# Kernel tuning notes

Measured on AMD Instinct MI355X. Metric: run time of the kernel, lower is better.

Reference implementation:

```python
import jax, jax.numpy as jnp
import numpy as np

NEIGHBOUR_NUM = 8  # args.neighbour_num


def _sqrdis_map(x, y):
    # x: [B,M,3], y: [B,N,3] -> [B,M,N] squared distances
    x2 = jnp.sum(x * x, axis=-1)
    y2 = jnp.sum(y * y, axis=-1)
    inner = jnp.einsum('bmd,bnd->bmn', x, y)
    return x2[:, :, None] + y2[:, None, :] - 2.0 * inner


def _chamfer(x, y):
    d = _sqrdis_map(x, y)
    return d.min(axis=2), d.min(axis=1)


def _neighbor_index(v, k):
    # torch.topk(dist, k+1, largest=False) then drop self
    d = _sqrdis_map(v, v)
    idx = jax.lax.top_k(-d, k + 1)[1]  # ascending distance order
    return idx[:, :, 1:]


def _arap(idx, dp, sp):
    B = dp.shape[0]
    bid = jnp.arange(B)[:, None, None]
    dn = dp[bid, idx] - dp[:, :, None, :]  # [B,N,K,3]
    sn = sp[bid, idx] - sp[:, :, None, :]
    dd = jnp.sqrt(jnp.sum(dn * dn, axis=-1) + 1e-5)
    sd = jnp.sqrt(jnp.sum(sn * sn, axis=-1) + 1e-5)
    diff = dd - sd
    return jnp.sum(diff * diff) / B


def setup_inputs() -> dict:
    key = jax.random.key(0)
    ks = jax.random.split(key, 7)
    T, B, N = 3, 4, 4096
    return {
        'phi': jax.random.normal(ks[0], (T, B, 1024), dtype=jnp.float32),
        'point_weight': jax.random.normal(ks[1], (T, B, N, 1), dtype=jnp.float32),
        'deform_rigid_points': 0.5 * jax.random.normal(ks[2], (T, B, N, 3), dtype=jnp.float32),
        'deformation_points': 0.5 * jax.random.normal(ks[3], (T, B, N, 3), dtype=jnp.float32),
        'rigid_matrix': 0.1 * jax.random.normal(ks[4], (T, B, 4, 4), dtype=jnp.float32),
        'source_points': jax.random.uniform(ks[5], (B, N, 3), dtype=jnp.float32, minval=-1.0, maxval=1.0),
        'target_points': jax.random.uniform(ks[6], (B, N, 3), dtype=jnp.float32, minval=-1.0, maxval=1.0),
    }


def reference(phi, point_weight, deform_rigid_points, deformation_points,
              rigid_matrix, source_points, target_points):
    B = source_points.shape[0]
    T = phi.shape[0]  # iter_time = len(phi_list)
    idx = _neighbor_index(source_points, NEIGHBOUR_NUM)
    trans_mask = jnp.zeros((4, 4), dtype=rigid_matrix.dtype).at[0:3, 3].set(1.0)
    total = jnp.asarray(0.0, dtype=source_points.dtype)
    for t in range(T):  # small fixed iter count, structurally distinct stages
        dp = deformation_points[t]
        # loss_on_cd
        d1, d2 = _chamfer(dp, target_points)
        cd = (jnp.sum(d1) + jnp.sum(d2)) * 0.5 / B
        # loss_on_pd (rigid-deformed vs full deformation)
        diff = deform_rigid_points[t] - dp
        pd = jnp.sum(diff * diff) / B
        # loss_on_sparse
        sp = jnp.mean(jnp.abs(point_weight[t]))
        # loss_on_tran
        tr = trans_mask[None] * rigid_matrix[t]
        tran = jnp.sum(tr * tr) / B
        # loss_on_arap
        ar = _arap(idx, dp, source_points)
        total = total + cd + pd + sp + tran + ar
    return total
```

## Files before the change

kernel.cpp:

```cpp
#include <hip/hip_runtime.h>

#define T_ 3
#define B_ 4
#define N_ 4096
#define K_ 8

#define GROUPS 32
#define GRP_KNN 32
#define GRP_CH  12
#define GRP_SZ  45
#define CWIN 512

typedef short bf16x8 __attribute__((ext_vector_type(8)));
typedef float f32x4  __attribute__((ext_vector_type(4)));

template <int NW>
__device__ inline float block_reduce(float v, float* scratch) {
    #pragma unroll
    for (int off = 32; off > 0; off >>= 1) v += __shfl_down(v, off, 64);
    const int lane = threadIdx.x & 63, wid = threadIdx.x >> 6;
    if (lane == 0) scratch[wid] = v;
    __syncthreads();
    float s = 0.f;
    if (threadIdx.x == 0) {
        #pragma unroll
        for (int w = 0; w < NW; ++w) s += scratch[w];
    }
    return s;
}

#define CE_(A, i, j) { unsigned lo_ = min(A[i], A[j]); A[j] = max(A[i], A[j]); A[i] = lo_; }
__device__ inline void sort8(unsigned s[8]) {
    CE_(s,0,1) CE_(s,2,3) CE_(s,4,5) CE_(s,6,7)
    CE_(s,0,2) CE_(s,1,3) CE_(s,4,6) CE_(s,5,7)
    CE_(s,1,2) CE_(s,5,6)
    CE_(s,0,4) CE_(s,1,5) CE_(s,2,6) CE_(s,3,7)
    CE_(s,2,4) CE_(s,3,5)
    CE_(s,1,2) CE_(s,3,4) CE_(s,5,6)
}
__device__ inline void merge_top8(unsigned a[8], const unsigned s[8]) {
    #pragma unroll
    for (int i = 0; i < 8; ++i) a[i] = min(a[i], s[7 - i]);
    CE_(a,0,4) CE_(a,1,5) CE_(a,2,6) CE_(a,3,7)
    CE_(a,0,2) CE_(a,1,3) CE_(a,4,6) CE_(a,5,7)
    CE_(a,0,1) CE_(a,2,3) CE_(a,4,5) CE_(a,6,7)
}

__device__ inline short hi16(float v) { return (short)(__float_as_uint(v) >> 16); }
__device__ inline float residual(float v) {
    return v - __uint_as_float(__float_as_uint(v) & 0xFFFF0000u);
}
__device__ inline unsigned pk2(short a, short b) {
    return (unsigned)(unsigned short)a | ((unsigned)(unsigned short)b << 16);
}
#define BF16_ONE ((short)0x3F80)

__global__ __launch_bounds__(256, 6) void mega_kernel(const float* __restrict__ src,
                                                      const float* __restrict__ dp_all,
                                                      const float* __restrict__ tp,
                                                      const float* __restrict__ drp,
                                                      const float* __restrict__ pw,
                                                      const float* __restrict__ rm,
                                                      float* __restrict__ out) {
    __shared__ uint4 smem4[1024];
    const f32x4 zero4 = {0.f, 0.f, 0.f, 0.f};

    const int g = blockIdx.x / GRP_SZ;
    const int r = blockIdx.x % GRP_SZ;

    if (r < GRP_KNN) {
        const int knn_id = g * GRP_KNN + r;
        uint4* alds = smem4;
        const int b   = knn_id / (N_ / 16);
        const int qt0 = (knn_id % (N_ / 16)) * 16;
        const float* sb = src + (size_t)b * N_ * 3;

        const int wid  = __builtin_amdgcn_readfirstlane(threadIdx.x >> 6);
        const int lane = threadIdx.x & 63;
        const int n    = lane & 15;
        const int quad = lane >> 4;
        const int rbase = quad * 4;
        const int qid  = qt0 + n;

        bf16x8 bfrag = (bf16x8)(short)0;
        {
            float x = sb[3 * qid], y = sb[3 * qid + 1], z = sb[3 * qid + 2];
            float q2 = fmaf(x, x, fmaf(y, y, z * z));
            short hx = hi16(x), hy = hi16(y), hz = hi16(z);
            short lx = hi16(residual(x)), ly = hi16(residual(y)), lz = hi16(residual(z));
            if (quad == 0) bfrag = (bf16x8){hx, hy, hz, hx, hy, hz, BF16_ONE, BF16_ONE};
            else if (quad == 1) bfrag = (bf16x8){lx, ly, lz, lx, ly, lz,
                                                 hi16(q2), hi16(residual(q2))};
        }

        unsigned a[K_];
        #pragma unroll
        for (int p = 0; p < K_; ++p) a[p] = 0xFFFFFFFFu;

        for (int w = 0; w < N_ / CWIN; ++w) {
            __syncthreads();
            #pragma unroll
            for (int rr = 0; rr < 2; ++rr) {
                int jloc = rr * 256 + threadIdx.x;
                int jg = w * CWIN + jloc;
                float x = sb[3 * jg], y = sb[3 * jg + 1], z = sb[3 * jg + 2];
                float p2 = fmaf(x, x, fmaf(y, y, z * z));
                float mx = -2.f * x, my = -2.f * y, mz = -2.f * z;
                short mhx = hi16(mx), mhy = hi16(my), mhz = hi16(mz);
                short mlx = hi16(residual(mx)), mly = hi16(residual(my)), mlz = hi16(residual(mz));
                uint4 f0 = make_uint4(pk2(mhx, mhy), pk2(mhz, mlx), pk2(mly, mlz),
                                      pk2(hi16(p2), hi16(residual(p2))));
                uint4 f1 = make_uint4(f0.x, f0.y, f0.z, pk2(BF16_ONE, BF16_ONE));
                int tile = jloc >> 4, m = jloc & 15;
                alds[tile * 32 + m]      = f0;
                alds[tile * 32 + 16 + m] = f1;
            }
            __syncthreads();

            #pragma unroll
            for (int bt = 0; bt < 4; ++bt) {
                unsigned s8[8];
                #pragma unroll
                for (int h = 0; h < 2; ++h) {
                    const int tile = wid * 8 + bt * 2 + h;
                    const int tbg  = w * CWIN + tile * 16;
                    bf16x8 af = (bf16x8)(short)0;
                    if (quad < 2) {
                        union { uint4 u; bf16x8 v; } cv;
                        cv.u = alds[tile * 32 + quad * 16 + n];
                        af = cv.v;
                    }
                    f32x4 d = __builtin_amdgcn_mfma_f32_16x16x32_bf16(af, bfrag, zero4, 0, 0, 0);
                    #pragma unroll
                    for (int rr = 0; rr < 4; ++rr)
                        s8[h * 4 + rr] = (__float_as_uint(d[rr]) & 0xFFFFF000u)
                                         | (unsigned)(tbg | (rbase + rr));
                    if (tbg == qt0) {
                        #pragma unroll
                        for (int rr = 0; rr < 4; ++rr)
                            if (rbase + rr == n) s8[h * 4 + rr] = 0xFFFFFFFFu;
                    }
                }
                sort8(s8);
                merge_top8(a, s8);
            }
        }

        #pragma unroll
        for (int mk = 16; mk <= 32; mk <<= 1) {
            unsigned t[8];
            #pragma unroll
            for (int e = 0; e < K_; ++e) t[e] = __shfl_xor(a[e], mk, 64);
            merge_top8(a, t);
        }

        __syncthreads();
        unsigned* sm = (unsigned*)smem4;
        unsigned* nidx = (unsigned*)smem4 + 1024;
        if (lane < 16) {
            #pragma unroll
            for (int e = 0; e < K_; ++e) sm[(wid * 16 + n) * 9 + e] = a[e];
        }
        __syncthreads();
        if (threadIdx.x < 16) {
            const int q = threadIdx.x;
            unsigned md[K_];
            #pragma unroll
            for (int e = 0; e < K_; ++e) md[e] = sm[q * 9 + e];
            #pragma unroll
            for (int wv = 1; wv < 4; ++wv) {
                unsigned t[8];
                #pragma unroll
                for (int e = 0; e < K_; ++e) t[e] = sm[(wv * 16 + q) * 9 + e];
                merge_top8(md, t);
            }
            #pragma unroll
            for (int e = 0; e < K_; ++e) nidx[q * 8 + e] = md[e] & 0xFFFu;
        }
        __syncthreads();

        float acc = 0.f;
        if (threadIdx.x < 16 * K_) {
            const int q  = threadIdx.x >> 3;
            const int qi = qt0 + q;
            const int j  = (int)nidx[threadIdx.x];
            float sx = sb[3 * qi], sy = sb[3 * qi + 1], sz = sb[3 * qi + 2];
            float ex = sb[3 * j] - sx, ey = sb[3 * j + 1] - sy, ez = sb[3 * j + 2] - sz;
            float sd = sqrtf(fmaf(ex, ex, fmaf(ey, ey, ez * ez)) + 1e-5f);
            #pragma unroll
            for (int t = 0; t < T_; ++t) {
                const float* dpb = dp_all + ((size_t)(t * B_ + b)) * N_ * 3;
                float dx = dpb[3 * j] - dpb[3 * qi];
                float dy = dpb[3 * j + 1] - dpb[3 * qi + 1];
                float dz = dpb[3 * j + 2] - dpb[3 * qi + 2];
                float dd = sqrtf(fmaf(dx, dx, fmaf(dy, dy, dz * dz)) + 1e-5f);
                float df = dd - sd;
                acc = fmaf(df, df, acc);
            }
        }
        float s = block_reduce<4>(acc, (float*)smem4);
        if (threadIdx.x == 0) atomicAdd(out, s * (1.0f / B_));

    } else if (r < GRP_KNN + GRP_CH) {
        const int cb = g * GRP_CH + (r - GRP_KNN);
        uint4* alds = smem4;
        const int tbd  = cb >> 4;
        const int slab = cb & 15;
        const int dir = tbd & 1;
        const int tb  = tbd >> 1;
        const int b = tb % B_, t = tb / B_;

        const float* dpb = dp_all + ((size_t)(t * B_ + b)) * N_ * 3;
        const float* tpb = tp + (size_t)b * N_ * 3;
        const float* cbase = dir ? dpb : tpb;
        const float* qbase = dir ? tpb : dpb;

        const int lane = threadIdx.x & 63;
        const int wave = threadIdx.x >> 6;
        const int quad = lane >> 4;
        const int n    = lane & 15;

        bf16x8 bfrag[4];
        float  q2r[4];
        #pragma unroll
        for (int s = 0; s < 4; ++s) {
            int qid = slab * 256 + wave * 64 + s * 16 + n;
            float x = qbase[3 * qid], y = qbase[3 * qid + 1], z = qbase[3 * qid + 2];
            q2r[s] = fmaf(x, x, fmaf(y, y, z * z));
            short hx = hi16(x), hy = hi16(y), hz = hi16(z);
            short lx = hi16(residual(x)), ly = hi16(residual(y)), lz = hi16(residual(z));
            if (quad == 0)
                bfrag[s] = (bf16x8){hx, hy, hz, hx, hy, hz, BF16_ONE, BF16_ONE};
            else if (quad == 1)
                bfrag[s] = (bf16x8){lx, ly, lz, lx, ly, lz, 0, 0};
            else
                bfrag[s] = (bf16x8)(short)0;
        }

        float run[4] = {3.4e38f, 3.4e38f, 3.4e38f, 3.4e38f};

        for (int w = 0; w < N_ / CWIN; ++w) {
            __syncthreads();
            #pragma unroll
            for (int rr = 0; rr < 2; ++rr) {
                int jloc = rr * 256 + threadIdx.x;
                int jg = w * CWIN + jloc;
                float x = cbase[3 * jg], y = cbase[3 * jg + 1], z = cbase[3 * jg + 2];
                float p2 = fmaf(x, x, fmaf(y, y, z * z));
                float mx = -2.f * x, my = -2.f * y, mz = -2.f * z;
                short mhx = hi16(mx), mhy = hi16(my), mhz = hi16(mz);
                short mlx = hi16(residual(mx)), mly = hi16(residual(my)), mlz = hi16(residual(mz));
                uint4 f0 = make_uint4(pk2(mhx, mhy), pk2(mhz, mlx), pk2(mly, mlz),
                                      pk2(hi16(p2), hi16(residual(p2))));
                uint4 f1 = make_uint4(f0.x, f0.y, f0.z, 0u);
                int tile = jloc >> 4, m = jloc & 15;
                alds[tile * 32 + m]      = f0;
                alds[tile * 32 + 16 + m] = f1;
            }
            __syncthreads();

            #pragma unroll 4
            for (int tile = 0; tile < CWIN / 16; ++tile) {
                bf16x8 af = (bf16x8)(short)0;
                if (quad < 2) {
                    union { uint4 u; bf16x8 v; } cv;
                    cv.u = alds[tile * 32 + quad * 16 + n];
                    af = cv.v;
                }
                #pragma unroll
                for (int s = 0; s < 4; ++s) {
                    f32x4 d = __builtin_amdgcn_mfma_f32_16x16x32_bf16(af, bfrag[s], zero4, 0, 0, 0);
                    float r3 = fminf(fminf(d[0], d[1]), d[2]);
                    run[s] = fminf(fminf(run[s], r3), d[3]);
                }
            }
        }

        float vsum = 0.f;
        #pragma unroll
        for (int s = 0; s < 4; ++s) {
            float rr = run[s];
            rr = fminf(rr, __shfl_xor(rr, 32));
            rr = fminf(rr, __shfl_xor(rr, 16));
            if (lane < 16) vsum += rr + q2r[s];
        }
        __syncthreads();
        float ssum = block_reduce<4>(vsum, (float*)smem4);
        if (threadIdx.x == 0) atomicAdd(out, ssum * (0.5f / B_));

    } else {
        const int PD_N = T_ * B_ * N_ * 3;
        const int SP_N = T_ * B_ * N_;
        const int stride = GROUPS * 256;
        const int gid = g * 256 + threadIdx.x;
        float apd = 0.f;
        for (int i = gid; i < PD_N; i += stride) {
            float d = drp[i] - dp_all[i];
            apd = fmaf(d, d, apd);
        }
        float asp = 0.f;
        for (int i = gid; i < SP_N; i += stride) asp += fabsf(pw[i]);
        float atr = 0.f;
        if (gid < T_ * B_ * 3) {
            int t = gid / (B_ * 3);
            int b = (gid / 3) % B_;
            int rr = gid % 3;
            float v = rm[t * B_ * 16 + b * 16 + rr * 4 + 3];
            atr = v * v;
        }
        float acc = apd * (1.0f / B_) + asp * (1.0f / (B_ * N_)) + atr * (1.0f / B_);
        float s = block_reduce<4>(acc, (float*)smem4);
        if (threadIdx.x == 0) atomicAdd(out, s);
    }
}

extern "C" void kernel_launch(void* const* d_in, const int* in_sizes, int n_in,
                              void* d_out, int out_size, void* d_ws, size_t ws_size,
                              hipStream_t stream) {
    const float* pw  = (const float*)d_in[1];
    const float* drp = (const float*)d_in[2];
    const float* dp  = (const float*)d_in[3];
    const float* rm  = (const float*)d_in[4];
    const float* sp  = (const float*)d_in[5];
    const float* tp  = (const float*)d_in[6];
    float* out = (float*)d_out;

    hipMemsetAsync(out, 0, sizeof(float), stream);
    mega_kernel<<<GROUPS * GRP_SZ, 256, 0, stream>>>(sp, dp, tp, drp, pw, rm, out);
}
```

Measured before the change: 122.8 us.

## Switch chamfer MFMA to 32x32x16 and fold query norm into K

The chamfer branch moves from 16x16x32 bf16 MFMAs, where half of the K dimension was zero padding, to 32x32x16 MFMAs with a fully packed K. The hi/lo split coordinates, the candidate norm and the query norm now all sit inside the dot product, so the query norm no longer has to be added after the reduction. This halves the per-wave query fragments and doubles useful work per MFMA, meant to cut wasted matrix throughput and min-reduction VALU per distance. The LDS layout changes to two 512-entry K-halves, and the fully unrolled 16-tile loop may raise register pressure.

```diff
diff --git a/kernel.cpp b/kernel.cpp
--- a/kernel.cpp
+++ b/kernel.cpp
@@ -13,6 +13,7 @@
 
 typedef short bf16x8 __attribute__((ext_vector_type(8)));
 typedef float f32x4  __attribute__((ext_vector_type(4)));
+typedef float f32x16 __attribute__((ext_vector_type(16)));
 
 template <int NW>
 __device__ inline float block_reduce(float v, float* scratch) {
@@ -202,8 +203,10 @@
         if (threadIdx.x == 0) atomicAdd(out, s * (1.0f / B_));
 
     } else if (r < GRP_KNN + GRP_CH) {
+        const f32x16 zero16 = {0.f,0.f,0.f,0.f, 0.f,0.f,0.f,0.f,
+                               0.f,0.f,0.f,0.f, 0.f,0.f,0.f,0.f};
+        uint4* alds = smem4;
         const int cb = g * GRP_CH + (r - GRP_KNN);
-        uint4* alds = smem4;
         const int tbd  = cb >> 4;
         const int slab = cb & 15;
         const int dir = tbd & 1;
@@ -216,74 +219,69 @@
         const float* qbase = dir ? tpb : dpb;
 
         const int lane = threadIdx.x & 63;
-        const int wave = threadIdx.x >> 6;
-        const int quad = lane >> 4;
-        const int n    = lane & 15;
-
-        bf16x8 bfrag[4];
-        float  q2r[4];
+        const int wid  = __builtin_amdgcn_readfirstlane(threadIdx.x >> 6);
+        const int col  = lane & 31;
+        const int kg   = lane >> 5;
+
+        bf16x8 bfrag[2];
         #pragma unroll
-        for (int s = 0; s < 4; ++s) {
-            int qid = slab * 256 + wave * 64 + s * 16 + n;
+        for (int s = 0; s < 2; ++s) {
+            const int qid = slab * 256 + s * 128 + wid * 32 + col;
             float x = qbase[3 * qid], y = qbase[3 * qid + 1], z = qbase[3 * qid + 2];
-            q2r[s] = fmaf(x, x, fmaf(y, y, z * z));
+            float q2 = fmaf(x, x, fmaf(y, y, z * z));
             short hx = hi16(x), hy = hi16(y), hz = hi16(z);
             short lx = hi16(residual(x)), ly = hi16(residual(y)), lz = hi16(residual(z));
-            if (quad == 0)
-                bfrag[s] = (bf16x8){hx, hy, hz, hx, hy, hz, BF16_ONE, BF16_ONE};
-            else if (quad == 1)
-                bfrag[s] = (bf16x8){lx, ly, lz, lx, ly, lz, 0, 0};
-            else
-                bfrag[s] = (bf16x8)(short)0;
-        }
-
-        float run[4] = {3.4e38f, 3.4e38f, 3.4e38f, 3.4e38f};
+            if (kg == 0) bfrag[s] = (bf16x8){hx, hy, hz, hx, hy, hz, lx, ly};
+            else bfrag[s] = (bf16x8){lz, lx, ly, lz, BF16_ONE, BF16_ONE,
+                                     hi16(q2), hi16(residual(q2))};
+        }
+
+        float run0 = 3.4e38f, run1 = 3.4e38f;
 
         for (int w = 0; w < N_ / CWIN; ++w) {
             __syncthreads();
             #pragma unroll
             for (int rr = 0; rr < 2; ++rr) {
-                int jloc = rr * 256 + threadIdx.x;
-                int jg = w * CWIN + jloc;
+                int j = rr * 256 + (int)threadIdx.x;
+                int jg = w * CWIN + j;
                 float x = cbase[3 * jg], y = cbase[3 * jg + 1], z = cbase[3 * jg + 2];
                 float p2 = fmaf(x, x, fmaf(y, y, z * z));
                 float mx = -2.f * x, my = -2.f * y, mz = -2.f * z;
                 short mhx = hi16(mx), mhy = hi16(my), mhz = hi16(mz);
                 short mlx = hi16(residual(mx)), mly = hi16(residual(my)), mlz = hi16(residual(mz));
-                uint4 f0 = make_uint4(pk2(mhx, mhy), pk2(mhz, mlx), pk2(mly, mlz),
-                                      pk2(hi16(p2), hi16(residual(p2))));
-                uint4 f1 = make_uint4(f0.x, f0.y, f0.z, 0u);
-                int tile = jloc >> 4, m = jloc & 15;
-                alds[tile * 32 + m]      = f0;
-                alds[tile * 32 + 16 + m] = f1;
+                unsigned w0 = pk2(mhx, mhy), w1 = pk2(mhz, mlx), w2 = pk2(mly, mlz);
+                unsigned pw2 = pk2(hi16(p2), hi16(residual(p2)));
+                alds[j]       = make_uint4(w0, w1, w2, w0);
+                alds[512 + j] = make_uint4(w1, w2, pw2, pk2(BF16_ONE, BF16_ONE));
             }
             __syncthreads();
 
-            #pragma unroll 4
-            for (int tile = 0; tile < CWIN / 16; ++tile) {
-                bf16x8 af = (bf16x8)(short)0;
-                if (quad < 2) {
-                    union { uint4 u; bf16x8 v; } cv;
-                    cv.u = alds[tile * 32 + quad * 16 + n];
-                    af = cv.v;
+            #pragma unroll
+            for (int tile = 0; tile < CWIN / 32; ++tile) {
+                union { uint4 u; bf16x8 v; } cv;
+                cv.u = alds[kg * 512 + tile * 32 + col];
+                {
+                    f32x16 d = __builtin_amdgcn_mfma_f32_32x32x16_bf16(cv.v, bfrag[0], zero16, 0, 0, 0);
+                    float m0 = fminf(fminf(d[0],  d[1]),  fminf(d[2],  d[3]));
+                    float m1 = fminf(fminf(d[4],  d[5]),  fminf(d[6],  d[7]));
+                    float m2 = fminf(fminf(d[8],  d[9]),  fminf(d[10], d[11]));
+                    float m3 = fminf(fminf(d[12], d[13]), fminf(d[14], d[15]));
+                    run0 = fminf(run0, fminf(fminf(m0, m1), fminf(m2, m3)));
                 }
-                #pragma unroll
-                for (int s = 0; s < 4; ++s) {
-                    f32x4 d = __builtin_amdgcn_mfma_f32_16x16x32_bf16(af, bfrag[s], zero4, 0, 0, 0);
-                    float r3 = fminf(fminf(d[0], d[1]), d[2]);
-                    run[s] = fminf(fminf(run[s], r3), d[3]);
+                {
+                    f32x16 d = __builtin_amdgcn_mfma_f32_32x32x16_bf16(cv.v, bfrag[1], zero16, 0, 0, 0);
+                    float m0 = fminf(fminf(d[0],  d[1]),  fminf(d[2],  d[3]));
+                    float m1 = fminf(fminf(d[4],  d[5]),  fminf(d[6],  d[7]));
+                    float m2 = fminf(fminf(d[8],  d[9]),  fminf(d[10], d[11]));
+                    float m3 = fminf(fminf(d[12], d[13]), fminf(d[14], d[15]));
+                    run1 = fminf(run1, fminf(fminf(m0, m1), fminf(m2, m3)));
                 }
             }
         }
 
-        float vsum = 0.f;
-        #pragma unroll
-        for (int s = 0; s < 4; ++s) {
-            float rr = run[s];
-            rr = fminf(rr, __shfl_xor(rr, 32));
-            rr = fminf(rr, __shfl_xor(rr, 16));
-            if (lane < 16) vsum += rr + q2r[s];
-        }
+        run0 = fminf(run0, __shfl_xor(run0, 32, 64));
+        run1 = fminf(run1, __shfl_xor(run1, 32, 64));
+        float vsum = (lane < 32) ? (run0 + run1) : 0.f;
         __syncthreads();
         float ssum = block_reduce<4>(vsum, (float*)smem4);
         if (threadIdx.x == 0) atomicAdd(out, ssum * (0.5f / B_));
```

Measured after the change: 121.9 us. Within noise of the previous version (-0.7%).
